# Performance work log

Measured on AMD Instinct MI355X. Metric: run time of the kernel, lower is better.

## Reference

```python
import jax, jax.numpy as jnp
import numpy as np
from jax import lax


def _fps(xyz, num_group):
    """Farthest point sampling. xyz: (B, N, 3) -> centers (B, G, 3).
    Sequential over G (structural loop) via lax.scan; starts at index 0."""
    B, N, _ = xyz.shape

    def step(carry, _):
        min_d, last_idx = carry                      # (B, N), (B,)
        last_pt = jax.vmap(lambda p, i: p[i])(xyz, last_idx)  # (B, 3)
        d = jnp.sum((xyz - last_pt[:, None, :]) ** 2, axis=-1)  # (B, N)
        min_d = jnp.minimum(min_d, d)
        nxt = jnp.argmax(min_d, axis=-1).astype(jnp.int32)
        return (min_d, nxt), last_idx

    init = (jnp.full((B, N), jnp.inf, dtype=xyz.dtype),
            jnp.zeros((B,), dtype=jnp.int32))
    _, idxs = lax.scan(step, init, None, length=num_group)  # (G, B)
    idxs = idxs.T                                            # (B, G)
    centers = jax.vmap(lambda p, i: p[i])(xyz, idxs)         # (B, G, 3)
    return centers


def setup_inputs() -> dict:
    key = jax.random.key(0)
    xyz = jax.random.normal(key, (32, 8192, 3), dtype=jnp.float32)
    return {"xyz": xyz, "num_group": 256, "group_size": 32}


def reference(xyz, num_group, group_size):
    B, N, C = xyz.shape
    center = _fps(xyz, num_group)                            # (B, G, 3)
    # dense pairwise distances: (B, G, N)
    dist = jnp.linalg.norm(center[:, :, None, :] - xyz[:, None, :, :], axis=-1)
    _, idx = lax.top_k(-dist, group_size)                    # (B, G, k) smallest dists
    # gather neighbors per batch: (B, G, k, 3)
    patch = jax.vmap(lambda pts, i: pts[i])(xyz, idx)
    patch = patch - center[:, :, None, :]                    # recenter
    return (patch, center)
```

## Files before the change

### kernel.cpp

```cpp
#include <hip/hip_runtime.h>

#pragma clang fp contract(off)

#define BB 32
#define NN 8192
#define GG 256
#define KK 32

#define TFPS 512
#define JPF (NN / TFPS)

template <int CTRL>
__device__ __forceinline__ float rot_maxf(float v) {
  const int o =
      __builtin_amdgcn_update_dpp(0, __float_as_int(v), CTRL, 0xF, 0xF, true);
  return fmaxf(v, __int_as_float(o));
}

__global__ __launch_bounds__(TFPS, 1) void fps_kernel(const float* __restrict__ xyz,
                                                      float* __restrict__ out) {
#pragma clang fp contract(off)
  const int b = blockIdx.x;
  const int t = threadIdx.x;
  const int lane = t & 63;
  const int wave = t >> 6;
  const float* __restrict__ P = xyz + (size_t)b * NN * 3;

  __shared__ float4 pts[NN];
  __shared__ float rowmax[2][32];
  __shared__ unsigned winIdx[2];

  float px[JPF], py[JPF], pz[JPF], md[JPF];
#pragma unroll
  for (int j = 0; j < JPF; ++j) {
    const int idx = t + j * TFPS;
    const float x = P[idx * 3 + 0];
    const float y = P[idx * 3 + 1];
    const float z = P[idx * 3 + 2];
    px[j] = x; py[j] = y; pz[j] = z;
    md[j] = __builtin_inff();
    pts[idx] = make_float4(x, y, z, 0.0f);
  }
  if (t == 0) { winIdx[0] = 0xFFFFFFFFu; winIdx[1] = 0xFFFFFFFFu; }
  __syncthreads();

  unsigned win = 0;
  unsigned mywin = 0;

  for (int i = 0; i < GG; ++i) {
    if (t == i) mywin = win;
    if (i == GG - 1) break;

    const float4 c = pts[win];
    const float cx = c.x, cy = c.y, cz = c.z;

    float bv = -1.0f;
#pragma unroll
    for (int j = 0; j < JPF; ++j) {
      const float dx = px[j] - cx;
      const float dy = py[j] - cy;
      const float dz = pz[j] - cz;
      const float d = dx * dx + dy * dy + dz * dz;
      const float m = md[j] < d ? md[j] : d;
      md[j] = m;
      bv = fmaxf(bv, m);
    }

    float r = bv;
    r = rot_maxf<0x121>(r);
    r = rot_maxf<0x122>(r);
    r = rot_maxf<0x124>(r);
    r = rot_maxf<0x128>(r);
    if ((lane & 15) == 0)
      rowmax[i & 1][wave * 4 + (lane >> 4)] = r;
    __syncthreads();

    if (t == 0) winIdx[(i + 1) & 1] = 0xFFFFFFFFu;

    const float* __restrict__ rm = rowmax[i & 1];
    const int g = lane & 15;
    float m2 = fmaxf(rm[g], rm[g + 16]);
    m2 = rot_maxf<0x121>(m2);
    m2 = rot_maxf<0x122>(m2);
    m2 = rot_maxf<0x124>(m2);
    m2 = rot_maxf<0x128>(m2);
    const float M = m2;

    if (bv == M) {
      int fj = 0;
#pragma unroll
      for (int j = JPF - 1; j >= 0; --j)
        if (md[j] == M) fj = j;
      atomicMin(&winIdx[i & 1], (unsigned)t + ((unsigned)fj << 9));
    }
    __syncthreads();

    win = winIdx[i & 1];
  }

  if (t < GG) {
    const float4 c = pts[mywin];
    float* __restrict__ co =
        out + (size_t)BB * GG * KK * 3 + ((size_t)b * GG + t) * 3;
    co[0] = c.x; co[1] = c.y; co[2] = c.z;
  }
}

__global__ __launch_bounds__(512, 1) void knn_kernel(const float* __restrict__ xyz,
                                                     float* __restrict__ out) {
#pragma clang fp contract(off)
  const int b = blockIdx.x >> 3;
  const int chunk = blockIdx.x & 7;
  const int t = threadIdx.x;
  const int lane = t & 63;
  const int wave = t >> 6;
  const float* __restrict__ P = xyz + (size_t)b * NN * 3;

  __shared__ float xs[NN], ys[NN], zs[NN];
  __shared__ unsigned long long cand[8][256];

  for (int pt = t; pt < NN; pt += 512) {
    xs[pt] = P[pt * 3 + 0];
    ys[pt] = P[pt * 3 + 1];
    zs[pt] = P[pt * 3 + 2];
  }
  __syncthreads();

  const float* __restrict__ cent = out + (size_t)BB * GG * KK * 3;

  for (int gi = 0; gi < 4; ++gi) {
    const int g = chunk * 32 + wave * 4 + gi;
    const float cx = cent[((size_t)b * GG + g) * 3 + 0];
    const float cy = cent[((size_t)b * GG + g) * 3 + 1];
    const float cz = cent[((size_t)b * GG + g) * 3 + 2];

    float d2r[128];
    float mn = __builtin_inff();
#pragma unroll
    for (int j = 0; j < 128; ++j) {
      const int idx = lane + j * 64;
      const float dx = xs[idx] - cx;
      const float dy = ys[idx] - cy;
      const float dz = zs[idx] - cz;
      const float d2 = dx * dx + dy * dy + dz * dz;
      d2r[j] = d2;
      mn = fminf(mn, d2);
    }

    float sm = mn;
#pragma unroll
    for (int k = 2; k <= 64; k <<= 1) {
#pragma unroll
      for (int j2 = k >> 1; j2 > 0; j2 >>= 1) {
        const float o = __shfl_xor(sm, j2, 64);
        const bool keepMin = (((lane & k) == 0) == ((lane & j2) == 0));
        sm = keepMin ? fminf(sm, o) : fmaxf(sm, o);
      }
    }
    const float v = __shfl(sm, 31, 64);
    const float vi = __uint_as_float(__float_as_uint(v) + 8);

    unsigned cnt = 0;
    unsigned long long* __restrict__ cb = cand[wave];
#pragma unroll
    for (int j = 0; j < 128; ++j) {
      const bool p = d2r[j] <= vi;
      const unsigned long long mk = __ballot(p);
      if (p) {
        const unsigned off = cnt + (unsigned)__popcll(mk & ((1ull << lane) - 1));
        if (off < 256)
          cb[off] = ((unsigned long long)__float_as_uint(d2r[j]) << 32) |
                    (unsigned)(lane + j * 64);
      }
      cnt += (unsigned)__popcll(mk);
    }
    if (cnt > 256) cnt = 256;

    auto conv = [](unsigned long long e) -> unsigned long long {
      const float d = sqrtf(__uint_as_float((unsigned)(e >> 32)));
      return ((unsigned long long)__float_as_uint(d) << 32) | (e & 0xFFFFFFFFull);
    };

    unsigned long long myk;
    if (cnt <= 64) {
      unsigned long long key = ~0ull;
      if ((unsigned)lane < cnt) key = conv(cb[lane]);
#pragma unroll
      for (int k = 2; k <= 64; k <<= 1) {
#pragma unroll
        for (int j2 = k >> 1; j2 > 0; j2 >>= 1) {
          const unsigned long long o = __shfl_xor(key, j2, 64);
          const bool keepMin = (((lane & k) == 0) == ((lane & j2) == 0));
          const unsigned long long lo = o < key ? o : key;
          const unsigned long long hi = o < key ? key : o;
          key = keepMin ? lo : hi;
        }
      }
      myk = key;
    } else {
      unsigned long long k0 = ~0ull, k1 = ~0ull, k2 = ~0ull, k3 = ~0ull;
      if ((unsigned)lane < cnt)         k0 = conv(cb[lane]);
      if ((unsigned)(lane + 64) < cnt)  k1 = conv(cb[lane + 64]);
      if ((unsigned)(lane + 128) < cnt) k2 = conv(cb[lane + 128]);
      if ((unsigned)(lane + 192) < cnt) k3 = conv(cb[lane + 192]);
      unsigned long long got = ~0ull;
      for (int r = 0; r < 32; ++r) {
        unsigned long long m01 = k0 < k1 ? k0 : k1;
        unsigned long long m23 = k2 < k3 ? k2 : k3;
        unsigned long long m = m01 < m23 ? m01 : m23;
#pragma unroll
        for (int s = 32; s > 0; s >>= 1) {
          const unsigned long long o = __shfl_xor(m, s, 64);
          m = o < m ? o : m;
        }
        if (lane == r) got = m;
        if (k0 == m) k0 = ~0ull;
        else if (k1 == m) k1 = ~0ull;
        else if (k2 == m) k2 = ~0ull;
        else if (k3 == m) k3 = ~0ull;
      }
      myk = got;
    }

    if (lane < KK) {
      const unsigned idx = (unsigned)(myk & 0xFFFFFFFFull);
      const float ox = xs[idx] - cx;
      const float oy = ys[idx] - cy;
      const float oz = zs[idx] - cz;
      float* __restrict__ po = out + ((size_t)(((size_t)b * GG + g) * KK + lane)) * 3;
      po[0] = ox; po[1] = oy; po[2] = oz;
    }
  }
}

extern "C" void kernel_launch(void* const* d_in, const int* in_sizes, int n_in,
                              void* d_out, int out_size, void* d_ws, size_t ws_size,
                              hipStream_t stream) {
  const float* xyz = (const float*)d_in[0];
  float* out = (float*)d_out;
  fps_kernel<<<dim3(BB), dim3(TFPS), 0, stream>>>(xyz, out);
  knn_kernel<<<dim3(BB * 8), dim3(512), 0, stream>>>(xyz, out);
}
```

Baseline: 339.1 us.

## Batch four centers per point load in KNN and recompute distances

The KNN kernel stores points as float4 in shared memory, so each point is read with one wide LDS load instead of three scalar loads. The min-distance pass now handles all four centers of a wave at once, reusing each point load across four distance computations. The 128-entry per-lane distance register array is dropped, and distances are recomputed in the candidate-collection pass. This cuts register pressure and shared-memory traffic at the cost of computing the distances twice.

```diff
diff --git a/kernel.cpp b/kernel.cpp
--- a/kernel.cpp
+++ b/kernel.cpp
@@ -116,37 +116,53 @@
   const int wave = t >> 6;
   const float* __restrict__ P = xyz + (size_t)b * NN * 3;
 
-  __shared__ float xs[NN], ys[NN], zs[NN];
+  __shared__ float4 pts4[NN];
   __shared__ unsigned long long cand[8][256];
 
-  for (int pt = t; pt < NN; pt += 512) {
-    xs[pt] = P[pt * 3 + 0];
-    ys[pt] = P[pt * 3 + 1];
-    zs[pt] = P[pt * 3 + 2];
-  }
+  for (int pt = t; pt < NN; pt += 512)
+    pts4[pt] = make_float4(P[pt * 3 + 0], P[pt * 3 + 1], P[pt * 3 + 2], 0.0f);
   __syncthreads();
 
   const float* __restrict__ cent = out + (size_t)BB * GG * KK * 3;
-
-  for (int gi = 0; gi < 4; ++gi) {
-    const int g = chunk * 32 + wave * 4 + gi;
-    const float cx = cent[((size_t)b * GG + g) * 3 + 0];
-    const float cy = cent[((size_t)b * GG + g) * 3 + 1];
-    const float cz = cent[((size_t)b * GG + g) * 3 + 2];
-
-    float d2r[128];
-    float mn = __builtin_inff();
-#pragma unroll
-    for (int j = 0; j < 128; ++j) {
-      const int idx = lane + j * 64;
-      const float dx = xs[idx] - cx;
-      const float dy = ys[idx] - cy;
-      const float dz = zs[idx] - cz;
-      const float d2 = dx * dx + dy * dy + dz * dz;
-      d2r[j] = d2;
-      mn = fminf(mn, d2);
-    }
-
+  const int gbase = chunk * 32 + wave * 4;
+
+  const float c0x = cent[((size_t)b * GG + gbase + 0) * 3 + 0];
+  const float c0y = cent[((size_t)b * GG + gbase + 0) * 3 + 1];
+  const float c0z = cent[((size_t)b * GG + gbase + 0) * 3 + 2];
+  const float c1x = cent[((size_t)b * GG + gbase + 1) * 3 + 0];
+  const float c1y = cent[((size_t)b * GG + gbase + 1) * 3 + 1];
+  const float c1z = cent[((size_t)b * GG + gbase + 1) * 3 + 2];
+  const float c2x = cent[((size_t)b * GG + gbase + 2) * 3 + 0];
+  const float c2y = cent[((size_t)b * GG + gbase + 2) * 3 + 1];
+  const float c2z = cent[((size_t)b * GG + gbase + 2) * 3 + 2];
+  const float c3x = cent[((size_t)b * GG + gbase + 3) * 3 + 0];
+  const float c3y = cent[((size_t)b * GG + gbase + 3) * 3 + 1];
+  const float c3z = cent[((size_t)b * GG + gbase + 3) * 3 + 2];
+
+  float mn0 = __builtin_inff(), mn1 = __builtin_inff();
+  float mn2 = __builtin_inff(), mn3 = __builtin_inff();
+#pragma unroll 4
+  for (int j = 0; j < 128; ++j) {
+    const float4 p = pts4[lane + j * 64];
+    {
+      const float dx = p.x - c0x, dy = p.y - c0y, dz = p.z - c0z;
+      mn0 = fminf(mn0, dx * dx + dy * dy + dz * dz);
+    }
+    {
+      const float dx = p.x - c1x, dy = p.y - c1y, dz = p.z - c1z;
+      mn1 = fminf(mn1, dx * dx + dy * dy + dz * dz);
+    }
+    {
+      const float dx = p.x - c2x, dy = p.y - c2y, dz = p.z - c2z;
+      mn2 = fminf(mn2, dx * dx + dy * dy + dz * dz);
+    }
+    {
+      const float dx = p.x - c3x, dy = p.y - c3y, dz = p.z - c3z;
+      mn3 = fminf(mn3, dx * dx + dy * dy + dz * dz);
+    }
+  }
+
+  auto thresh = [&](float mn) -> float {
     float sm = mn;
 #pragma unroll
     for (int k = 2; k <= 64; k <<= 1) {
@@ -158,19 +174,29 @@
       }
     }
     const float v = __shfl(sm, 31, 64);
-    const float vi = __uint_as_float(__float_as_uint(v) + 8);
-
+    return __uint_as_float(__float_as_uint(v) + 8);
+  };
+  const float vi0 = thresh(mn0);
+  const float vi1 = thresh(mn1);
+  const float vi2 = thresh(mn2);
+  const float vi3 = thresh(mn3);
+
+  auto dogroup = [&](int g, float cx, float cy, float cz, float vi) {
     unsigned cnt = 0;
     unsigned long long* __restrict__ cb = cand[wave];
-#pragma unroll
+#pragma unroll 4
     for (int j = 0; j < 128; ++j) {
-      const bool p = d2r[j] <= vi;
-      const unsigned long long mk = __ballot(p);
-      if (p) {
+      const int idx = lane + j * 64;
+      const float4 p = pts4[idx];
+      const float dx = p.x - cx, dy = p.y - cy, dz = p.z - cz;
+      const float d2 = dx * dx + dy * dy + dz * dz;
+      const bool pr = d2 <= vi;
+      const unsigned long long mk = __ballot(pr);
+      if (pr) {
         const unsigned off = cnt + (unsigned)__popcll(mk & ((1ull << lane) - 1));
         if (off < 256)
-          cb[off] = ((unsigned long long)__float_as_uint(d2r[j]) << 32) |
-                    (unsigned)(lane + j * 64);
+          cb[off] = ((unsigned long long)__float_as_uint(d2) << 32) |
+                    (unsigned)idx;
       }
       cnt += (unsigned)__popcll(mk);
     }
@@ -224,13 +250,17 @@
 
     if (lane < KK) {
       const unsigned idx = (unsigned)(myk & 0xFFFFFFFFull);
-      const float ox = xs[idx] - cx;
-      const float oy = ys[idx] - cy;
-      const float oz = zs[idx] - cz;
-      float* __restrict__ po = out + ((size_t)(((size_t)b * GG + g) * KK + lane)) * 3;
-      po[0] = ox; po[1] = oy; po[2] = oz;
-    }
-  }
+      const float4 p = pts4[idx];
+      float* __restrict__ po =
+          out + ((size_t)(((size_t)b * GG + g) * KK + lane)) * 3;
+      po[0] = p.x - cx; po[1] = p.y - cy; po[2] = p.z - cz;
+    }
+  };
+
+  dogroup(gbase + 0, c0x, c0y, c0z, vi0);
+  dogroup(gbase + 1, c1x, c1y, c1z, vi1);
+  dogroup(gbase + 2, c2x, c2y, c2z, vi2);
+  dogroup(gbase + 3, c3x, c3y, c3z, vi3);
 }
 
 extern "C" void kernel_launch(void* const* d_in, const int* in_sizes, int n_in,
```

Result: faster. 319.2 us (median of 4 runs) (-5.8%).
